# Kernel tuning notes

Measured on AMD Instinct MI355X. Metric: run time of the kernel, lower is better.

Reference implementation:

```python
import jax, jax.numpy as jnp
import numpy as np


def setup_inputs() -> dict:
    key = jax.random.key(0)
    k1, k2, k3, k4 = jax.random.split(key, 4)
    N, M, D = 4096, 4096, 1024
    H = jax.random.normal(k1, (N, D), dtype=jnp.float32)
    K = jax.random.normal(k2, (M, D), dtype=jnp.float32)
    V = jax.random.normal(k3, (M, D), dtype=jnp.float32)
    attn_mask = jax.random.uniform(k4, (N, M), dtype=jnp.float32)
    return {"H": H, "K": K, "V": V, "attn_mask": attn_mask}


def reference(H, K, V, attn_mask):
    # scores: [N, M] = H @ K^T, scaled by sqrt(d)
    d = H.shape[1]
    scores = jnp.matmul(H, K.T) / jnp.sqrt(jnp.asarray(d, dtype=H.dtype))
    # double softmax with elementwise mask multiply in between
    probs = jax.nn.softmax(jax.nn.softmax(scores, axis=1) * attn_mask, axis=1)
    return jnp.matmul(probs, V)
```

## Files before the change

kernel.cpp:

```cpp
#include <hip/hip_runtime.h>
#include <cstdint>

typedef unsigned short u16;
typedef __bf16 bf16x8 __attribute__((ext_vector_type(8)));
typedef float f32x4 __attribute__((ext_vector_type(4)));
typedef unsigned int u32x4 __attribute__((ext_vector_type(4)));

__device__ __forceinline__ float bf2f(u16 h) {
  union { unsigned int u; float f; } v; v.u = ((unsigned int)h) << 16; return v.f;
}
__device__ __forceinline__ u16 f2bf(float f) {
  union { float f; unsigned int u; } v; v.f = f;
  unsigned int u = v.u;
  return (u16)((u + 0x7FFFu + ((u >> 16) & 1u)) >> 16);
}

__device__ __forceinline__ void ld_lds16(const void* g, void* l) {
  __builtin_amdgcn_global_load_lds(
      (const __attribute__((address_space(1))) unsigned int*)g,
      (__attribute__((address_space(3))) unsigned int*)l, 16, 0, 0);
}

__global__ __launch_bounds__(256) void gemm1_kernel(
    const u16* __restrict__ A, const u16* __restrict__ B,
    u16* __restrict__ S, float* __restrict__ L1, int ldA, int ldB, int ldC)
{
  __shared__ u16 smem[128 * 136];
  u16* As = smem;
  u16* Bs = smem + 8192;

  const int tid  = threadIdx.x;
  const int lane = tid & 63;
  const int w    = tid >> 6;
  const int wr   = w >> 1;
  const int wc   = w & 1;
  const int quad = lane >> 4;
  const int cIn  = lane & 15;

  const int flat = blockIdx.x;
  const int xcd  = flat & 7;
  const int i    = flat >> 3;
  const int rowBlk = ((xcd >> 2) * 16 + (i & 15)) * 128;
  const int colBlk = ((xcd & 3) * 8 + (i >> 4)) * 128;

  const int lrow   = lane >> 3;
  const int gchunk = (lane & 7) ^ lrow;

  f32x4 acc[4][4];
  #pragma unroll
  for (int a = 0; a < 4; ++a)
    #pragma unroll
    for (int b = 0; b < 4; ++b) acc[a][b] = {0.f, 0.f, 0.f, 0.f};

  for (int k0 = 0; k0 < 1024; k0 += 64) {
    #pragma unroll
    for (int t = 0; t < 4; ++t) {
      int rg = w * 4 + t;
      const u16* ga = A + (size_t)(rowBlk + rg * 8 + lrow) * ldA + k0 + gchunk * 8;
      const u16* gb = B + (size_t)(colBlk + rg * 8 + lrow) * ldB + k0 + gchunk * 8;
      ld_lds16(ga, &As[rg * 512]);
      ld_lds16(gb, &Bs[rg * 512]);
    }
    __syncthreads();

    #pragma unroll
    for (int ks = 0; ks < 2; ++ks) {
      bf16x8 af[4], bfr[4];
      #pragma unroll
      for (int mi = 0; mi < 4; ++mi) {
        int row = wr * 64 + mi * 16 + cIn;
        int ch  = (ks * 4 + quad) ^ (row & 7);
        af[mi]  = *(const bf16x8*)&As[row * 64 + ch * 8];
      }
      #pragma unroll
      for (int ni = 0; ni < 4; ++ni) {
        int row = wc * 64 + ni * 16 + cIn;
        int ch  = (ks * 4 + quad) ^ (row & 7);
        bfr[ni] = *(const bf16x8*)&Bs[row * 64 + ch * 8];
      }
      #pragma unroll
      for (int mi = 0; mi < 4; ++mi)
        #pragma unroll
        for (int ni = 0; ni < 4; ++ni)
          acc[mi][ni] = __builtin_amdgcn_mfma_f32_16x16x32_bf16(
              af[mi], bfr[ni], acc[mi][ni], 0, 0, 0);
    }
    __syncthreads();
  }

  const float scale = 0.03125f;
  #pragma unroll
  for (int mi = 0; mi < 4; ++mi) {
    float rs[4] = {0.f, 0.f, 0.f, 0.f};
    #pragma unroll
    for (int ni = 0; ni < 4; ++ni) {
      int colT = wc * 64 + ni * 16 + cIn;
      #pragma unroll
      for (int r = 0; r < 4; ++r) {
        int rowT = wr * 64 + mi * 16 + quad * 4 + r;
        u16 sb = f2bf(acc[mi][ni][r] * scale);
        smem[rowT * 136 + colT] = sb;
        rs[r] += __expf(bf2f(sb));
      }
    }
    #pragma unroll
    for (int m = 1; m < 16; m <<= 1)
      #pragma unroll
      for (int r = 0; r < 4; ++r) rs[r] += __shfl_xor(rs[r], m, 64);
    if (cIn == 0) {
      #pragma unroll
      for (int r = 0; r < 4; ++r)
        atomicAdd(&L1[rowBlk + wr * 64 + mi * 16 + quad * 4 + r], rs[r]);
    }
  }
  __syncthreads();
  #pragma unroll
  for (int it = 0; it < 8; ++it) {
    int j  = it * 256 + tid;
    int r  = j >> 4;
    int c8 = j & 15;
    u32x4 v = *(const u32x4*)&smem[r * 136 + c8 * 8];
    __builtin_nontemporal_store(
        v, (u32x4*)&S[(size_t)(rowBlk + r) * ldC + colBlk + c8 * 8]);
  }
}

__global__ __launch_bounds__(256) void gemm2_kernel(
    const u16* __restrict__ A, const u16* __restrict__ B,
    float* __restrict__ Out, const float* __restrict__ L2,
    int ldA, int ldB, int ldC)
{
  __shared__ u16 As[64 * 64];
  __shared__ u16 Bs[128 * 64];

  const int tid  = threadIdx.x;
  const int lane = tid & 63;
  const int w    = tid >> 6;
  const int wrow = w >> 1;
  const int wcol = w & 1;
  const int quad = lane >> 4;
  const int cIn  = lane & 15;

  const int flat = blockIdx.x;
  const int xcd  = flat & 7;
  const int i    = flat >> 3;
  const int rowBlk = (xcd * 8 + (i & 7)) * 64;
  const int colBlk = (i >> 3) * 128;

  const int lrow   = lane >> 3;
  const int gchunk = (lane & 7) ^ lrow;

  f32x4 acc[2][4];
  #pragma unroll
  for (int a = 0; a < 2; ++a)
    #pragma unroll
    for (int b = 0; b < 4; ++b) acc[a][b] = {0.f, 0.f, 0.f, 0.f};

  for (int k0 = 0; k0 < 4096; k0 += 64) {
    #pragma unroll
    for (int t = 0; t < 2; ++t) {
      int rg = w * 2 + t;
      const u16* ga = A + (size_t)(rowBlk + rg * 8 + lrow) * ldA + k0 + gchunk * 8;
      ld_lds16(ga, &As[rg * 512]);
    }
    #pragma unroll
    for (int t = 0; t < 4; ++t) {
      int rg = w * 4 + t;
      const u16* gb = B + (size_t)(colBlk + rg * 8 + lrow) * ldB + k0 + gchunk * 8;
      ld_lds16(gb, &Bs[rg * 512]);
    }
    __syncthreads();

    #pragma unroll
    for (int ks = 0; ks < 2; ++ks) {
      bf16x8 af[2], bfr[4];
      #pragma unroll
      for (int mi = 0; mi < 2; ++mi) {
        int row = wrow * 32 + mi * 16 + cIn;
        int ch  = (ks * 4 + quad) ^ (row & 7);
        af[mi]  = *(const bf16x8*)&As[row * 64 + ch * 8];
      }
      #pragma unroll
      for (int ni = 0; ni < 4; ++ni) {
        int row = wcol * 64 + ni * 16 + cIn;
        int ch  = (ks * 4 + quad) ^ (row & 7);
        bfr[ni] = *(const bf16x8*)&Bs[row * 64 + ch * 8];
      }
      #pragma unroll
      for (int mi = 0; mi < 2; ++mi)
        #pragma unroll
        for (int ni = 0; ni < 4; ++ni)
          acc[mi][ni] = __builtin_amdgcn_mfma_f32_16x16x32_bf16(
              af[mi], bfr[ni], acc[mi][ni], 0, 0, 0);
    }
    __syncthreads();
  }

  #pragma unroll
  for (int mi = 0; mi < 2; ++mi) {
    #pragma unroll
    for (int r = 0; r < 4; ++r) {
      int row   = rowBlk + wrow * 32 + mi * 16 + quad * 4 + r;
      float inv = 1.0f / L2[row];
      #pragma unroll
      for (int ni = 0; ni < 4; ++ni) {
        int col = colBlk + wcol * 64 + ni * 16 + cIn;
        __builtin_nontemporal_store(acc[mi][ni][r] * inv,
                                    &Out[(size_t)row * ldC + col]);
      }
    }
  }
}

__global__ __launch_bounds__(256) void prep_kernel(
    const float* __restrict__ H, const float* __restrict__ Kin,
    const float* __restrict__ V, u16* __restrict__ Hb, u16* __restrict__ Kb,
    u16* __restrict__ Vt, float* __restrict__ L1)
{
  int b = blockIdx.x;
  if (b < 8192) {
    const float* src = (b < 4096) ? H : Kin;
    u16* dst = (b < 4096) ? Hb : Kb;
    int i = (b & 4095) * 256 + threadIdx.x;
    float4 v = ((const float4*)src)[i];
    ushort4 o;
    o.x = f2bf(v.x); o.y = f2bf(v.y); o.z = f2bf(v.z); o.w = f2bf(v.w);
    ((ushort4*)dst)[i] = o;
  } else if (b < 12288) {
    __shared__ float tile[32][33];
    b -= 8192;
    int c0 = (b & 31) * 32;
    int r0 = (b >> 5) * 32;
    int tx = threadIdx.x & 31, ty = threadIdx.x >> 5;
    #pragma unroll
    for (int s = 0; s < 32; s += 8)
      tile[ty + s][tx] = V[(size_t)(r0 + ty + s) * 1024 + c0 + tx];
    __syncthreads();
    #pragma unroll
    for (int s = 0; s < 32; s += 8)
      Vt[(size_t)(c0 + ty + s) * 4096 + r0 + tx] = f2bf(tile[tx][ty + s]);
  } else {
    float4* z = (float4*)L1;
    #pragma unroll
    for (int q = 0; q < 8; ++q)
      z[q * 256 + threadIdx.x] = {0.f, 0.f, 0.f, 0.f};
  }
}

__global__ __launch_bounds__(256) void softmax2_kernel(
    u16* __restrict__ S, const float* __restrict__ mask,
    const float* __restrict__ L1, float* __restrict__ L2, int M)
{
  int row = blockIdx.x;
  float inv = 1.0f / L1[row];
  u16* srow = S + (size_t)row * M;
  const float* mrow = mask + (size_t)row * M;
  float lsum = 0.f;
  for (int base = threadIdx.x * 16; base < M; base += blockDim.x * 16) {
    u16 sl[16];
    *(uint4*)(sl)     = *(const uint4*)(srow + base);
    *(uint4*)(sl + 8) = *(const uint4*)(srow + base + 8);
    float mv[16];
    #pragma unroll
    for (int q = 0; q < 4; ++q)
      *(f32x4*)(mv + q * 4) =
          __builtin_nontemporal_load((const f32x4*)(mrow + base + q * 4));
    #pragma unroll
    for (int j = 0; j < 16; ++j) {
      float t = __expf(bf2f(sl[j])) * inv * mv[j];
      float p = __expf(t);
      lsum += p;
      sl[j] = f2bf(p);
    }
    *(uint4*)(srow + base)     = *(uint4*)(sl);
    *(uint4*)(srow + base + 8) = *(uint4*)(sl + 8);
  }
  #pragma unroll
  for (int m = 1; m < 64; m <<= 1) lsum += __shfl_xor(lsum, m, 64);
  __shared__ float wred[4];
  if ((threadIdx.x & 63) == 0) wred[threadIdx.x >> 6] = lsum;
  __syncthreads();
  if (threadIdx.x == 0) L2[row] = wred[0] + wred[1] + wred[2] + wred[3];
}

extern "C" void kernel_launch(void* const* d_in, const int* in_sizes, int n_in,
                              void* d_out, int out_size, void* d_ws, size_t ws_size,
                              hipStream_t stream) {
  const float* H    = (const float*)d_in[0];
  const float* Kin  = (const float*)d_in[1];
  const float* V    = (const float*)d_in[2];
  const float* mask = (const float*)d_in[3];
  float* out = (float*)d_out;

  const int N = 4096, M = 4096, D = 1024;

  char* ws = (char*)d_ws;
  u16*   Hb = (u16*)(ws);
  u16*   Kb = (u16*)(ws + (8ull << 20));
  u16*   Vt = (u16*)(ws + (16ull << 20));
  u16*   S  = (u16*)(ws + (24ull << 20));
  float* L1 = (float*)(ws + (56ull << 20));
  float* L2 = (float*)(ws + (56ull << 20) + 16384);

  prep_kernel<<<dim3(12289), dim3(256), 0, stream>>>(H, Kin, V, Hb, Kb, Vt, L1);

  gemm1_kernel<<<dim3(1024), dim3(256), 0, stream>>>(Hb, Kb, S, L1, D, D, M);

  softmax2_kernel<<<dim3(N), dim3(256), 0, stream>>>(S, mask, L1, L2, M);

  gemm2_kernel<<<dim3(512), dim3(256), 0, stream>>>(S, Vt, out, L2, M, M, D);
}
```

Baseline: 255.4 us.

## Move first softmax row-sum into softmax kernel and double gemm2 K-tile

The first softmax's row sums are no longer built with atomics in the gemm1 epilogue. The softmax kernel now holds each full row in registers and computes both sums there, with one thread per 16 elements. The gemm1 epilogue now stages 16-row bands through a smaller LDS buffer and uses regular stores instead of nontemporal ones, which lowers LDS use and may raise occupancy. gemm2 now loads two 64-wide K slices per barrier, which halves the number of syncs. The L1 zeroing block in prep goes away, but the softmax kernel now assumes M equals 4096 exactly.

```diff
diff --git a/kernel.cpp b/kernel.cpp
--- a/kernel.cpp
+++ b/kernel.cpp
@@ -23,11 +23,12 @@
 
 __global__ __launch_bounds__(256) void gemm1_kernel(
     const u16* __restrict__ A, const u16* __restrict__ B,
-    u16* __restrict__ S, float* __restrict__ L1, int ldA, int ldB, int ldC)
+    u16* __restrict__ S, int ldA, int ldB, int ldC)
 {
-  __shared__ u16 smem[128 * 136];
+  __shared__ u16 smem[128 * 64 * 2];
   u16* As = smem;
   u16* Bs = smem + 8192;
+  u16* epi = smem;
 
   const int tid  = threadIdx.x;
   const int lane = tid & 63;
@@ -91,37 +92,26 @@
   const float scale = 0.03125f;
   #pragma unroll
   for (int mi = 0; mi < 4; ++mi) {
-    float rs[4] = {0.f, 0.f, 0.f, 0.f};
     #pragma unroll
     for (int ni = 0; ni < 4; ++ni) {
       int colT = wc * 64 + ni * 16 + cIn;
       #pragma unroll
       for (int r = 0; r < 4; ++r) {
-        int rowT = wr * 64 + mi * 16 + quad * 4 + r;
-        u16 sb = f2bf(acc[mi][ni][r] * scale);
-        smem[rowT * 136 + colT] = sb;
-        rs[r] += __expf(bf2f(sb));
-      }
-    }
-    #pragma unroll
-    for (int m = 1; m < 16; m <<= 1)
-      #pragma unroll
-      for (int r = 0; r < 4; ++r) rs[r] += __shfl_xor(rs[r], m, 64);
-    if (cIn == 0) {
-      #pragma unroll
-      for (int r = 0; r < 4; ++r)
-        atomicAdd(&L1[rowBlk + wr * 64 + mi * 16 + quad * 4 + r], rs[r]);
-    }
-  }
-  __syncthreads();
-  #pragma unroll
-  for (int it = 0; it < 8; ++it) {
-    int j  = it * 256 + tid;
-    int r  = j >> 4;
-    int c8 = j & 15;
-    u32x4 v = *(const u32x4*)&smem[r * 136 + c8 * 8];
-    __builtin_nontemporal_store(
-        v, (u32x4*)&S[(size_t)(rowBlk + r) * ldC + colBlk + c8 * 8]);
+        int band = wr * 16 + quad * 4 + r;
+        epi[band * 136 + colT] = f2bf(acc[mi][ni][r] * scale);
+      }
+    }
+    __syncthreads();
+    #pragma unroll
+    for (int it = 0; it < 2; ++it) {
+      int j   = it * 256 + tid;
+      int rr  = j >> 4;
+      int c8  = j & 15;
+      int grow = rowBlk + (rr >> 4) * 64 + mi * 16 + (rr & 15);
+      u32x4 v = *(const u32x4*)&epi[rr * 136 + c8 * 8];
+      *(u32x4*)&S[(size_t)grow * ldC + colBlk + c8 * 8] = v;
+    }
+    __syncthreads();
   }
 }
 
@@ -130,8 +120,8 @@
     float* __restrict__ Out, const float* __restrict__ L2,
     int ldA, int ldB, int ldC)
 {
-  __shared__ u16 As[64 * 64];
-  __shared__ u16 Bs[128 * 64];
+  __shared__ u16 As[2 * 64 * 64];
+  __shared__ u16 Bs[2 * 128 * 64];
 
   const int tid  = threadIdx.x;
   const int lane = tid & 63;
@@ -156,42 +146,49 @@
     #pragma unroll
     for (int b = 0; b < 4; ++b) acc[a][b] = {0.f, 0.f, 0.f, 0.f};
 
-  for (int k0 = 0; k0 < 4096; k0 += 64) {
-    #pragma unroll
-    for (int t = 0; t < 2; ++t) {
-      int rg = w * 2 + t;
-      const u16* ga = A + (size_t)(rowBlk + rg * 8 + lrow) * ldA + k0 + gchunk * 8;
-      ld_lds16(ga, &As[rg * 512]);
-    }
-    #pragma unroll
-    for (int t = 0; t < 4; ++t) {
-      int rg = w * 4 + t;
-      const u16* gb = B + (size_t)(colBlk + rg * 8 + lrow) * ldB + k0 + gchunk * 8;
-      ld_lds16(gb, &Bs[rg * 512]);
-    }
-    __syncthreads();
-
-    #pragma unroll
-    for (int ks = 0; ks < 2; ++ks) {
-      bf16x8 af[2], bfr[4];
-      #pragma unroll
-      for (int mi = 0; mi < 2; ++mi) {
-        int row = wrow * 32 + mi * 16 + cIn;
-        int ch  = (ks * 4 + quad) ^ (row & 7);
-        af[mi]  = *(const bf16x8*)&As[row * 64 + ch * 8];
-      }
-      #pragma unroll
-      for (int ni = 0; ni < 4; ++ni) {
-        int row = wcol * 64 + ni * 16 + cIn;
-        int ch  = (ks * 4 + quad) ^ (row & 7);
-        bfr[ni] = *(const bf16x8*)&Bs[row * 64 + ch * 8];
-      }
-      #pragma unroll
-      for (int mi = 0; mi < 2; ++mi)
+  for (int k0 = 0; k0 < 4096; k0 += 128) {
+    #pragma unroll
+    for (int h = 0; h < 2; ++h) {
+      int kk = k0 + h * 64;
+      #pragma unroll
+      for (int t = 0; t < 2; ++t) {
+        int rg = w * 2 + t;
+        const u16* ga = A + (size_t)(rowBlk + rg * 8 + lrow) * ldA + kk + gchunk * 8;
+        ld_lds16(ga, &As[h * 4096 + rg * 512]);
+      }
+      #pragma unroll
+      for (int t = 0; t < 4; ++t) {
+        int rg = w * 4 + t;
+        const u16* gb = B + (size_t)(colBlk + rg * 8 + lrow) * ldB + kk + gchunk * 8;
+        ld_lds16(gb, &Bs[h * 8192 + rg * 512]);
+      }
+    }
+    __syncthreads();
+
+    #pragma unroll
+    for (int h = 0; h < 2; ++h) {
+      #pragma unroll
+      for (int ks = 0; ks < 2; ++ks) {
+        bf16x8 af[2], bfr[4];
         #pragma unroll
-        for (int ni = 0; ni < 4; ++ni)
-          acc[mi][ni] = __builtin_amdgcn_mfma_f32_16x16x32_bf16(
-              af[mi], bfr[ni], acc[mi][ni], 0, 0, 0);
+        for (int mi = 0; mi < 2; ++mi) {
+          int row = wrow * 32 + mi * 16 + cIn;
+          int ch  = (ks * 4 + quad) ^ (row & 7);
+          af[mi]  = *(const bf16x8*)&As[h * 4096 + row * 64 + ch * 8];
+        }
+        #pragma unroll
+        for (int ni = 0; ni < 4; ++ni) {
+          int row = wcol * 64 + ni * 16 + cIn;
+          int ch  = (ks * 4 + quad) ^ (row & 7);
+          bfr[ni] = *(const bf16x8*)&Bs[h * 8192 + row * 64 + ch * 8];
+        }
+        #pragma unroll
+        for (int mi = 0; mi < 2; ++mi)
+          #pragma unroll
+          for (int ni = 0; ni < 4; ++ni)
+            acc[mi][ni] = __builtin_amdgcn_mfma_f32_16x16x32_bf16(
+                af[mi], bfr[ni], acc[mi][ni], 0, 0, 0);
+      }
     }
     __syncthreads();
   }
@@ -215,7 +212,7 @@
 __global__ __launch_bounds__(256) void prep_kernel(
     const float* __restrict__ H, const float* __restrict__ Kin,
     const float* __restrict__ V, u16* __restrict__ Hb, u16* __restrict__ Kb,
-    u16* __restrict__ Vt, float* __restrict__ L1)
+    u16* __restrict__ Vt)
 {
   int b = blockIdx.x;
   if (b < 8192) {
@@ -226,7 +223,7 @@
     ushort4 o;
     o.x = f2bf(v.x); o.y = f2bf(v.y); o.z = f2bf(v.z); o.w = f2bf(v.w);
     ((ushort4*)dst)[i] = o;
-  } else if (b < 12288) {
+  } else {
     __shared__ float tile[32][33];
     b -= 8192;
     int c0 = (b & 31) * 32;
@@ -239,48 +236,54 @@
     #pragma unroll
     for (int s = 0; s < 32; s += 8)
       Vt[(size_t)(c0 + ty + s) * 4096 + r0 + tx] = f2bf(tile[tx][ty + s]);
-  } else {
-    float4* z = (float4*)L1;
-    #pragma unroll
-    for (int q = 0; q < 8; ++q)
-      z[q * 256 + threadIdx.x] = {0.f, 0.f, 0.f, 0.f};
   }
 }
 
 __global__ __launch_bounds__(256) void softmax2_kernel(
     u16* __restrict__ S, const float* __restrict__ mask,
-    const float* __restrict__ L1, float* __restrict__ L2, int M)
+    float* __restrict__ L2, int M)
 {
   int row = blockIdx.x;
-  float inv = 1.0f / L1[row];
   u16* srow = S + (size_t)row * M;
   const float* mrow = mask + (size_t)row * M;
+  const int base = threadIdx.x * 16;
+
+  u16 sl[16];
+  *(uint4*)(sl)     = *(const uint4*)(srow + base);
+  *(uint4*)(sl + 8) = *(const uint4*)(srow + base + 8);
+
+  float e[16];
+  float s1 = 0.f;
+  #pragma unroll
+  for (int j = 0; j < 16; ++j) { e[j] = __expf(bf2f(sl[j])); s1 += e[j]; }
+
+  __shared__ float wred[8];
+  #pragma unroll
+  for (int m = 1; m < 64; m <<= 1) s1 += __shfl_xor(s1, m, 64);
+  if ((threadIdx.x & 63) == 0) wred[threadIdx.x >> 6] = s1;
+  __syncthreads();
+  float inv = 1.0f / (wred[0] + wred[1] + wred[2] + wred[3]);
+
+  float mv[16];
+  #pragma unroll
+  for (int q = 0; q < 4; ++q)
+    *(float4*)(mv + q * 4) = *(const float4*)(mrow + base + q * 4);
+
   float lsum = 0.f;
-  for (int base = threadIdx.x * 16; base < M; base += blockDim.x * 16) {
-    u16 sl[16];
-    *(uint4*)(sl)     = *(const uint4*)(srow + base);
-    *(uint4*)(sl + 8) = *(const uint4*)(srow + base + 8);
-    float mv[16];
-    #pragma unroll
-    for (int q = 0; q < 4; ++q)
-      *(f32x4*)(mv + q * 4) =
-          __builtin_nontemporal_load((const f32x4*)(mrow + base + q * 4));
-    #pragma unroll
-    for (int j = 0; j < 16; ++j) {
-      float t = __expf(bf2f(sl[j])) * inv * mv[j];
-      float p = __expf(t);
-      lsum += p;
-      sl[j] = f2bf(p);
-    }
-    *(uint4*)(srow + base)     = *(uint4*)(sl);
-    *(uint4*)(srow + base + 8) = *(uint4*)(sl + 8);
-  }
+  #pragma unroll
+  for (int j = 0; j < 16; ++j) {
+    float p = __expf(e[j] * inv * mv[j]);
+    lsum += p;
+    sl[j] = f2bf(p);
+  }
+  *(uint4*)(srow + base)     = *(uint4*)(sl);
+  *(uint4*)(srow + base + 8) = *(uint4*)(sl + 8);
+
   #pragma unroll
   for (int m = 1; m < 64; m <<= 1) lsum += __shfl_xor(lsum, m, 64);
-  __shared__ float wred[4];
-  if ((threadIdx.x & 63) == 0) wred[threadIdx.x >> 6] = lsum;
+  if ((threadIdx.x & 63) == 0) wred[4 + (threadIdx.x >> 6)] = lsum;
   __syncthreads();
-  if (threadIdx.x == 0) L2[row] = wred[0] + wred[1] + wred[2] + wred[3];
+  if (threadIdx.x == 0) L2[row] = wred[4] + wred[5] + wred[6] + wred[7];
 }
 
 extern "C" void kernel_launch(void* const* d_in, const int* in_sizes, int n_in,
@@ -299,14 +302,13 @@
   u16*   Kb = (u16*)(ws + (8ull << 20));
   u16*   Vt = (u16*)(ws + (16ull << 20));
   u16*   S  = (u16*)(ws + (24ull << 20));
-  float* L1 = (float*)(ws + (56ull << 20));
-  float* L2 = (float*)(ws + (56ull << 20) + 16384);
-
-  prep_kernel<<<dim3(12289), dim3(256), 0, stream>>>(H, Kin, V, Hb, Kb, Vt, L1);
-
-  gemm1_kernel<<<dim3(1024), dim3(256), 0, stream>>>(Hb, Kb, S, L1, D, D, M);
-
-  softmax2_kernel<<<dim3(N), dim3(256), 0, stream>>>(S, mask, L1, L2, M);
+  float* L2 = (float*)(ws + (56ull << 20));
+
+  prep_kernel<<<dim3(12288), dim3(256), 0, stream>>>(H, Kin, V, Hb, Kb, Vt);
+
+  gemm1_kernel<<<dim3(1024), dim3(256), 0, stream>>>(Hb, Kb, S, D, D, M);
+
+  softmax2_kernel<<<dim3(N), dim3(256), 0, stream>>>(S, mask, L2, M);
 
   gemm2_kernel<<<dim3(512), dim3(256), 0, stream>>>(S, Vt, out, L2, M, M, D);
 }
```

New measurement: 233.7 us. 1.09x faster.
